# Kernel optimization log

Hardware: AMD Instinct MI355X
Metric: run time of the kernel (lower is better)

The kernel has to match this reference:

```python
import jax, jax.numpy as jnp
import numpy as np

BATCH = 65536
IN_FEATURES = 128
OUT_FEATURES = 128
GRID = 8  # initial_grid: number of RBF/spline basis centers per edge


def setup_inputs() -> dict:
    key = jax.random.key(0)
    k1, k2, k3 = jax.random.split(key, 3)
    x = jax.random.normal(k1, (BATCH, IN_FEATURES), dtype=jnp.float32)
    # Per-edge spline coefficients stacked: [out, in, grid]
    coeffs = jax.random.normal(k2, (OUT_FEATURES, IN_FEATURES, GRID), dtype=jnp.float32) * 0.1
    # Per-edge base (SiLU) weights stacked: [out, in]
    base_w = jax.random.normal(k3, (OUT_FEATURES, IN_FEATURES), dtype=jnp.float32) * 0.1
    # Shared uniform grid of RBF centers in [-1, 1]
    centers = jnp.linspace(-1.0, 1.0, GRID, dtype=jnp.float32)
    return {"x": x, "coeffs": coeffs, "base_w": base_w, "centers": centers}


def reference(x, coeffs, base_w, centers):
    # HybridBasisFunction per edge: base_w * silu(x) + sum_g coeffs[g] * exp(-((x-c_g)/w)^2)
    width = 2.0 / (GRID - 1)  # grid spacing
    # basis: [B, in, G]
    diff = (x[:, :, None] - centers[None, None, :]) / width
    basis = jnp.exp(-diff * diff)
    # Sum over all edges (j -> i): output[b, i] = sum_j phi_ij(x[b, j])
    out = jnp.einsum('big,oig->bo', basis, coeffs)
    out = out + jnp.einsum('bi,oi->bo', jax.nn.silu(x), base_w)
    return out
```

## Files before the change

### kernel.cpp

```cpp
#include <hip/hip_runtime.h>

typedef _Float16 f16x8  __attribute__((ext_vector_type(8)));
typedef float    f32x4  __attribute__((ext_vector_type(4)));
typedef float    f32x16 __attribute__((ext_vector_type(16)));

#define BATCH 65536
#define NIN   128
#define NOUT  128

#define L2E   1.4426950408889634f
#define SQL2E 1.2011224087864498f
#define EM2   0.1353352832366127f


__global__ __launch_bounds__(256) void kan_prep(const float* __restrict__ coeffs,
                                                const float* __restrict__ base_w,
                                                _Float16* __restrict__ W3) {
    int t = blockIdx.x * 256 + threadIdx.x;
    int ks   = t >> 8;
    int c    = t & 255;
    int nbb  = c >> 6;
    int lane = c & 63;
    int sub  = lane >> 5;
    int col  = nbb * 32 + (lane & 31);
    f16x8 v;
    if (ks < 64) {
        int g = ks >> 3, t2 = ks & 7;
        const float* src = coeffs + ((size_t)col * 128 + g * 16 + sub * 8 + t2) * 8;
#pragma unroll
        for (int e = 0; e < 8; ++e) v[e] = (_Float16)src[e];
    } else {
        const float* src = base_w + (size_t)col * 128 + (ks - 64) * 16 + sub * 8;
#pragma unroll
        for (int e = 0; e < 8; ++e) v[e] = (_Float16)src[e];
    }
    *(f16x8*)((char*)W3 + (size_t)t * 16) = v;
}

__device__ __forceinline__ void gll16(const void* g, void* l) {
    __builtin_amdgcn_global_load_lds(
        (const __attribute__((address_space(1))) unsigned int*)g,
        (__attribute__((address_space(3))) unsigned int*)l, 16, 0, 0);
}

__device__ __forceinline__ f16x8 basis8r(float t) {
    float u = t * SQL2E;
    float b = __builtin_amdgcn_exp2f(-(u * u));
    float r = __builtin_amdgcn_exp2f(__builtin_fmaf(t, 2.0f * L2E, -L2E));
    f16x8 o;
    o[0] = (_Float16)b;
#pragma unroll
    for (int g = 1; g < 8; ++g) {
        b = b * r;
        r = r * EM2;
        o[g] = (_Float16)b;
    }
    return o;
}

__device__ __forceinline__ float silu1(float xv) {
    float p = __builtin_amdgcn_exp2f(-xv * L2E);
    return xv * __builtin_amdgcn_rcpf(1.0f + p);
}

__global__ __launch_bounds__(256, 2) void kan_main(const float* __restrict__ x,
                                                   const float* __restrict__ centers,
                                                   const _Float16* __restrict__ W3,
                                                   float* __restrict__ out) {
    __shared__ _Float16 smem[2][16384];

    const int tid  = threadIdx.x;
    const int lane = tid & 63;
    const int w    = tid >> 6;
    const int wr   = w >> 1;
    const int wc   = w & 1;
    const int l31  = lane & 31;
    const int sub  = lane >> 5;
    const int row0 = blockIdx.x * 128 + wr * 64;
    const int col0 = wc * 64;

    const float* xp = x + (size_t)(row0 + l31) * NIN;

    f32x16 acc[2][2];
#pragma unroll
    for (int m = 0; m < 2; ++m)
#pragma unroll
        for (int nbb = 0; nbb < 2; ++nbb)
#pragma unroll
            for (int r = 0; r < 16; ++r) acc[m][nbb][r] = 0.f;

    const char* wbase = (const char*)W3;
#define STAGE(buf, grp)                                                         \
    do {                                                                        \
        const char* _s = wbase + (size_t)(grp) * 32768 + (size_t)tid * 16;      \
        char*       _d = (char*)&smem[(buf)][0] + (size_t)tid * 16;             \
        _Pragma("unroll")                                                       \
        for (int _i = 0; _i < 8; ++_i) gll16(_s + _i * 4096, _d + _i * 4096);   \
    } while (0)

    STAGE(0, 0);
    __syncthreads();

#pragma unroll
    for (int g = 0; g < 8; ++g) {
        const int cur = g & 1;
        STAGE(cur ^ 1, g + 1);
        f32x4 xv[2][2];
#pragma unroll
        for (int m = 0; m < 2; ++m) {
            const float* p = xp + (size_t)m * 32 * NIN + g * 16 + sub * 8;
            xv[m][0] = *(const f32x4*)p;
            xv[m][1] = *(const f32x4*)(p + 4);
        }
#pragma unroll
        for (int t2 = 0; t2 < 8; ++t2) {
            const char* bp = (const char*)&smem[cur][0] + t2 * 4096 + wc * 2048 + lane * 16;
            f16x8 b0 = *(const f16x8*)bp;
            f16x8 b1 = *(const f16x8*)(bp + 1024);
#pragma unroll
            for (int m = 0; m < 2; ++m) {
                float xs = (t2 < 4) ? xv[m][0][t2 & 3] : xv[m][1][t2 & 3];
                f16x8 a = basis8r(__builtin_fmaf(xs, 3.5f, 3.5f));
                acc[m][0] = __builtin_amdgcn_mfma_f32_32x32x16_f16(a, b0, acc[m][0], 0, 0, 0);
                acc[m][1] = __builtin_amdgcn_mfma_f32_32x32x16_f16(a, b1, acc[m][1], 0, 0, 0);
            }
        }
        __syncthreads();
    }

#pragma unroll
    for (int s = 0; s < 8; ++s) {
        const char* bp = (const char*)&smem[0][0] + s * 4096 + wc * 2048 + lane * 16;
        f16x8 b0 = *(const f16x8*)bp;
        f16x8 b1 = *(const f16x8*)(bp + 1024);
#pragma unroll
        for (int m = 0; m < 2; ++m) {
            const float* p = xp + (size_t)m * 32 * NIN + s * 16 + sub * 8;
            f32x4 v0 = *(const f32x4*)p;
            f32x4 v1 = *(const f32x4*)(p + 4);
            f16x8 a;
#pragma unroll
            for (int e = 0; e < 4; ++e) {
                a[e]     = (_Float16)silu1(v0[e]);
                a[4 + e] = (_Float16)silu1(v1[e]);
            }
            acc[m][0] = __builtin_amdgcn_mfma_f32_32x32x16_f16(a, b0, acc[m][0], 0, 0, 0);
            acc[m][1] = __builtin_amdgcn_mfma_f32_32x32x16_f16(a, b1, acc[m][1], 0, 0, 0);
        }
    }

#pragma unroll
    for (int m = 0; m < 2; ++m)
#pragma unroll
        for (int nbb = 0; nbb < 2; ++nbb)
#pragma unroll
            for (int r = 0; r < 16; ++r) {
                int crow = (r & 3) + 8 * (r >> 2) + 4 * sub;
                out[(size_t)(row0 + m * 32 + crow) * NOUT + col0 + nbb * 32 + l31] = acc[m][nbb][r];
            }
}

extern "C" void kernel_launch(void* const* d_in, const int* in_sizes, int n_in,
                              void* d_out, int out_size, void* d_ws, size_t ws_size,
                              hipStream_t stream) {
    const float* x       = (const float*)d_in[0];
    const float* coeffs  = (const float*)d_in[1];
    const float* base_w  = (const float*)d_in[2];
    const float* centers = (const float*)d_in[3];
    _Float16* W3 = (_Float16*)d_ws;

    kan_prep<<<dim3(72), dim3(256), 0, stream>>>(coeffs, base_w, W3);
    kan_main<<<dim3(BATCH / 128), dim3(256), 0, stream>>>(x, centers, W3, (float*)d_out);
}
```

Baseline: 45.62 us.

## Remap waves to 32 rows x 128 cols, prefetch x, use packed fp16 converts

Each wave now owns 32 batch rows and all 128 output columns instead of a 64x64 tile. Each basis expansion is computed once and reused across four MFMAs, where before the B fragments were shared across two row blocks. This halves the per-wave exp/basis arithmetic, which was duplicated across the two column waves, at the cost of more LDS reads of weights per MFMA. It also prefetches the next x slice one stage ahead and packs fp16 conversions with cvt_pkrtz, which switches rounding to round-toward-zero.

```diff
diff --git a/kernel.cpp b/kernel.cpp
--- a/kernel.cpp
+++ b/kernel.cpp
@@ -1,5 +1,6 @@
 #include <hip/hip_runtime.h>
 
+typedef __fp16   pk16x2 __attribute__((ext_vector_type(2)));
 typedef _Float16 f16x8  __attribute__((ext_vector_type(8)));
 typedef float    f32x4  __attribute__((ext_vector_type(4)));
 typedef float    f32x16 __attribute__((ext_vector_type(16)));
@@ -44,17 +45,23 @@
 }
 
 __device__ __forceinline__ f16x8 basis8r(float t) {
-    float u = t * SQL2E;
-    float b = __builtin_amdgcn_exp2f(-(u * u));
-    float r = __builtin_amdgcn_exp2f(__builtin_fmaf(t, 2.0f * L2E, -L2E));
+    float u  = t * SQL2E;
+    float b0 = __builtin_amdgcn_exp2f(-(u * u));
+    float r  = __builtin_amdgcn_exp2f(__builtin_fmaf(t, 2.0f * L2E, -L2E));
+    float b1 = b0 * r; r *= EM2;
+    float b2 = b1 * r; r *= EM2;
+    float b3 = b2 * r; r *= EM2;
+    float b4 = b3 * r; r *= EM2;
+    float b5 = b4 * r; r *= EM2;
+    float b6 = b5 * r; r *= EM2;
+    float b7 = b6 * r;
+    pk16x2 p0 = __builtin_amdgcn_cvt_pkrtz(b0, b1);
+    pk16x2 p1 = __builtin_amdgcn_cvt_pkrtz(b2, b3);
+    pk16x2 p2 = __builtin_amdgcn_cvt_pkrtz(b4, b5);
+    pk16x2 p3 = __builtin_amdgcn_cvt_pkrtz(b6, b7);
     f16x8 o;
-    o[0] = (_Float16)b;
-#pragma unroll
-    for (int g = 1; g < 8; ++g) {
-        b = b * r;
-        r = r * EM2;
-        o[g] = (_Float16)b;
-    }
+    o[0] = p0[0]; o[1] = p0[1]; o[2] = p1[0]; o[3] = p1[1];
+    o[4] = p2[0]; o[5] = p2[1]; o[6] = p3[0]; o[7] = p3[1];
     return o;
 }
 
@@ -72,22 +79,17 @@
     const int tid  = threadIdx.x;
     const int lane = tid & 63;
     const int w    = tid >> 6;
-    const int wr   = w >> 1;
-    const int wc   = w & 1;
     const int l31  = lane & 31;
     const int sub  = lane >> 5;
-    const int row0 = blockIdx.x * 128 + wr * 64;
-    const int col0 = wc * 64;
+    const int row0 = blockIdx.x * 128 + w * 32;
 
     const float* xp = x + (size_t)(row0 + l31) * NIN;
 
-    f32x16 acc[2][2];
+    f32x16 acc[4];
 #pragma unroll
-    for (int m = 0; m < 2; ++m)
+    for (int nbb = 0; nbb < 4; ++nbb)
 #pragma unroll
-        for (int nbb = 0; nbb < 2; ++nbb)
-#pragma unroll
-            for (int r = 0; r < 16; ++r) acc[m][nbb][r] = 0.f;
+        for (int r = 0; r < 16; ++r) acc[nbb][r] = 0.f;
 
     const char* wbase = (const char*)W3;
 #define STAGE(buf, grp)                                                         \
@@ -99,65 +101,69 @@
     } while (0)
 
     STAGE(0, 0);
+    f32x4 xa = *(const f32x4*)(xp + sub * 8);
+    f32x4 xb = *(const f32x4*)(xp + sub * 8 + 4);
     __syncthreads();
 
 #pragma unroll
     for (int g = 0; g < 8; ++g) {
         const int cur = g & 1;
         STAGE(cur ^ 1, g + 1);
-        f32x4 xv[2][2];
+        const int nxt = (g < 7) ? (g + 1) * 16 : 0;
+        f32x4 xa2 = *(const f32x4*)(xp + nxt + sub * 8);
+        f32x4 xb2 = *(const f32x4*)(xp + nxt + sub * 8 + 4);
+
+        f16x8 a[8];
 #pragma unroll
-        for (int m = 0; m < 2; ++m) {
-            const float* p = xp + (size_t)m * 32 * NIN + g * 16 + sub * 8;
-            xv[m][0] = *(const f32x4*)p;
-            xv[m][1] = *(const f32x4*)(p + 4);
-        }
+        for (int t2 = 0; t2 < 4; ++t2) a[t2]     = basis8r(__builtin_fmaf(xa[t2], 3.5f, 3.5f));
+#pragma unroll
+        for (int t2 = 0; t2 < 4; ++t2) a[4 + t2] = basis8r(__builtin_fmaf(xb[t2], 3.5f, 3.5f));
+
 #pragma unroll
         for (int t2 = 0; t2 < 8; ++t2) {
-            const char* bp = (const char*)&smem[cur][0] + t2 * 4096 + wc * 2048 + lane * 16;
-            f16x8 b0 = *(const f16x8*)bp;
-            f16x8 b1 = *(const f16x8*)(bp + 1024);
+            const char* bp = (const char*)&smem[cur][0] + t2 * 4096 + lane * 16;
 #pragma unroll
-            for (int m = 0; m < 2; ++m) {
-                float xs = (t2 < 4) ? xv[m][0][t2 & 3] : xv[m][1][t2 & 3];
-                f16x8 a = basis8r(__builtin_fmaf(xs, 3.5f, 3.5f));
-                acc[m][0] = __builtin_amdgcn_mfma_f32_32x32x16_f16(a, b0, acc[m][0], 0, 0, 0);
-                acc[m][1] = __builtin_amdgcn_mfma_f32_32x32x16_f16(a, b1, acc[m][1], 0, 0, 0);
+            for (int nbb = 0; nbb < 4; ++nbb) {
+                f16x8 b = *(const f16x8*)(bp + nbb * 1024);
+                acc[nbb] = __builtin_amdgcn_mfma_f32_32x32x16_f16(a[t2], b, acc[nbb], 0, 0, 0);
             }
         }
+        xa = xa2; xb = xb2;
         __syncthreads();
     }
 
 #pragma unroll
     for (int s = 0; s < 8; ++s) {
-        const char* bp = (const char*)&smem[0][0] + s * 4096 + wc * 2048 + lane * 16;
-        f16x8 b0 = *(const f16x8*)bp;
-        f16x8 b1 = *(const f16x8*)(bp + 1024);
+        f32x4 xa2, xb2;
+        if (s < 7) {
+            xa2 = *(const f32x4*)(xp + (s + 1) * 16 + sub * 8);
+            xb2 = *(const f32x4*)(xp + (s + 1) * 16 + sub * 8 + 4);
+        }
+        float s0 = silu1(xa[0]), s1 = silu1(xa[1]), s2 = silu1(xa[2]), s3 = silu1(xa[3]);
+        float s4 = silu1(xb[0]), s5 = silu1(xb[1]), s6 = silu1(xb[2]), s7 = silu1(xb[3]);
+        pk16x2 p0 = __builtin_amdgcn_cvt_pkrtz(s0, s1);
+        pk16x2 p1 = __builtin_amdgcn_cvt_pkrtz(s2, s3);
+        pk16x2 p2 = __builtin_amdgcn_cvt_pkrtz(s4, s5);
+        pk16x2 p3 = __builtin_amdgcn_cvt_pkrtz(s6, s7);
+        f16x8 a;
+        a[0] = p0[0]; a[1] = p0[1]; a[2] = p1[0]; a[3] = p1[1];
+        a[4] = p2[0]; a[5] = p2[1]; a[6] = p3[0]; a[7] = p3[1];
+        const char* bp = (const char*)&smem[0][0] + s * 4096 + lane * 16;
 #pragma unroll
-        for (int m = 0; m < 2; ++m) {
-            const float* p = xp + (size_t)m * 32 * NIN + s * 16 + sub * 8;
-            f32x4 v0 = *(const f32x4*)p;
-            f32x4 v1 = *(const f32x4*)(p + 4);
-            f16x8 a;
-#pragma unroll
-            for (int e = 0; e < 4; ++e) {
-                a[e]     = (_Float16)silu1(v0[e]);
-                a[4 + e] = (_Float16)silu1(v1[e]);
-            }
-            acc[m][0] = __builtin_amdgcn_mfma_f32_32x32x16_f16(a, b0, acc[m][0], 0, 0, 0);
-            acc[m][1] = __builtin_amdgcn_mfma_f32_32x32x16_f16(a, b1, acc[m][1], 0, 0, 0);
+        for (int nbb = 0; nbb < 4; ++nbb) {
+            f16x8 b = *(const f16x8*)(bp + nbb * 1024);
+            acc[nbb] = __builtin_amdgcn_mfma_f32_32x32x16_f16(a, b, acc[nbb], 0, 0, 0);
         }
+        if (s < 7) { xa = xa2; xb = xb2; }
     }
 
 #pragma unroll
-    for (int m = 0; m < 2; ++m)
+    for (int nbb = 0; nbb < 4; ++nbb)
 #pragma unroll
-        for (int nbb = 0; nbb < 2; ++nbb)
-#pragma unroll
-            for (int r = 0; r < 16; ++r) {
-                int crow = (r & 3) + 8 * (r >> 2) + 4 * sub;
-                out[(size_t)(row0 + m * 32 + crow) * NOUT + col0 + nbb * 32 + l31] = acc[m][nbb][r];
-            }
+        for (int r = 0; r < 16; ++r) {
+            int crow = (r & 3) + 8 * (r >> 2) + 4 * sub;
+            out[(size_t)(row0 + crow) * NOUT + nbb * 32 + l31] = acc[nbb][r];
+        }
 }
 
 extern "C" void kernel_launch(void* const* d_in, const int* in_sizes, int n_in,
```

Measured after the change: 37.07 us. 18.7% less time.
